# Kernel optimization log

Hardware: AMD Instinct MI355X
Metric: run time of the kernel (lower is better)

Reference implementation:

```python
import jax, jax.numpy as jnp
import numpy as np

B, T, D = 4, 4096, 1024
H = 16
DK = D // H
EPS = 1e-6


def _phi(x):
    return jax.nn.elu(x) + 1.0


def setup_inputs() -> dict:
    key = jax.random.key(0)
    ks = jax.random.split(key, 9)
    s = 1.0 / np.sqrt(D)
    return {
        "x": jax.random.normal(ks[0], (B, T, D), dtype=jnp.float32),
        "Wq": jax.random.uniform(ks[1], (D, D), jnp.float32, -s, s),
        "bq": jax.random.uniform(ks[2], (D,), jnp.float32, -s, s),
        "Wk": jax.random.uniform(ks[3], (D, D), jnp.float32, -s, s),
        "bk": jax.random.uniform(ks[4], (D,), jnp.float32, -s, s),
        "Wv": jax.random.uniform(ks[5], (D, D), jnp.float32, -s, s),
        "bv": jax.random.uniform(ks[6], (D,), jnp.float32, -s, s),
        "Wo": jax.random.uniform(ks[7], (D, D), jnp.float32, -s, s),
        "bo": jax.random.uniform(ks[8], (D,), jnp.float32, -s, s),
    }


def reference(x, Wq, bq, Wk, bk, Wv, bv, Wo, bo):
    Bq, Tq, _ = x.shape

    def heads(y):  # [B,T,D] -> [B,H,T,DK]
        return y.reshape(Bq, Tq, H, DK).transpose(0, 2, 1, 3)

    q = _phi(heads(x @ Wq.T + bq))
    k = _phi(heads(x @ Wk.T + bk))
    v = heads(x @ Wv.T + bv)

    # associative KV summary: [B,H,DK,DK]
    kv = jnp.einsum("bhtd,bhtm->bhdm", k, v)
    # normalizer: q . (sum_t k + eps), then +eps, reciprocal
    z = 1.0 / (jnp.einsum("bhtd,bhd->bht", q, k.sum(axis=2) + EPS) + EPS)
    out = jnp.einsum("bhtd,bhdm,bht->bhtm", q, kv, z)

    out = out.transpose(0, 2, 1, 3).reshape(Bq, Tq, -1)  # [B,T,D]
    return out @ Wo.T + bo
```

## Files before the change

kernel.cpp:

```cpp
#include <hip/hip_runtime.h>
#include <cstdint>
#include <cstddef>

typedef unsigned short u16;
typedef __bf16 bf16x8 __attribute__((ext_vector_type(8)));
typedef float  f32x4  __attribute__((ext_vector_type(4)));
typedef u16    u16x8v __attribute__((ext_vector_type(8)));
typedef u16    u16x4  __attribute__((ext_vector_type(4)));

#define EPS 1e-6f

__device__ __forceinline__ u16 f2bf(float f) {
  union { float f; unsigned int u; } v; v.f = f;
  unsigned int u = v.u + 0x7FFFu + ((v.u >> 16) & 1u);
  return (u16)(u >> 16);
}
__device__ __forceinline__ float bf2f(u16 h) {
  union { unsigned int u; float f; } v; v.u = ((unsigned int)h) << 16;
  return v.f;
}
__device__ __forceinline__ void async16(const void* g, void* l) {
  __builtin_amdgcn_global_load_lds(
      (const __attribute__((address_space(1))) void*)g,
      (__attribute__((address_space(3))) void*)l, 16, 0, 0);
}

__global__ __launch_bounds__(256) void cvt_all_kernel(
    const float* __restrict__ x,
    const float* __restrict__ w0, const float* __restrict__ w1,
    const float* __restrict__ w2, const float* __restrict__ w3,
    u16* __restrict__ xb, u16* __restrict__ o0, u16* __restrict__ o1,
    u16* __restrict__ o2, u16* __restrict__ o3) {
  const int gb = blockIdx.x;
  const float* in;
  u16* out;
  int i;
  if (gb < 8192) {
    in = x; out = xb; i = gb * 256 + threadIdx.x;
  } else {
    const int wb = gb - 8192;
    in  = (wb < 512) ? w0 : (wb < 1024) ? w1 : (wb < 1536) ? w2 : w3;
    out = (wb < 512) ? o0 : (wb < 1024) ? o1 : (wb < 1536) ? o2 : o3;
    i = (wb & 511) * 256 + threadIdx.x;
  }
  const float4* p = (const float4*)in;
  float4 a = p[2 * (size_t)i], b = p[2 * (size_t)i + 1];
  u16x8v o;
  o[0] = f2bf(a.x); o[1] = f2bf(a.y); o[2] = f2bf(a.z); o[3] = f2bf(a.w);
  o[4] = f2bf(b.x); o[5] = f2bf(b.y); o[6] = f2bf(b.z); o[7] = f2bf(b.w);
  *(u16x8v*)(out + 8 * (size_t)i) = o;
}

template <int MODE>
__global__ __launch_bounds__(512) void gemm8g(
    const u16* __restrict__ A, const u16* __restrict__ Bw,
    const float* __restrict__ bias0, const float* __restrict__ bias1,
    const float* __restrict__ bias2,
    u16* __restrict__ O0, u16* __restrict__ O1, u16* __restrict__ O2,
    float* __restrict__ Of, int K) {
  __shared__ u16 sA[2][256 * 64];
  __shared__ u16 sB[2][256 * 64];

  const int tid = threadIdx.x, wave = tid >> 6, lane = tid & 63;
  const int bm = blockIdx.x * 256, bn = blockIdx.y * 256;
  const int wmh = (wave >> 2) * 64;
  const int wq  = (wave & 3) * 32;
  const int l15 = lane & 15, l4 = lane >> 4, l7 = lane & 7;

  f32x4 acc[8][4] = {};

  const int trow = tid >> 3;
  const int sch8 = ((tid & 7) ^ (trow & 7)) * 8;

#define STG_A(buf, qm, s, kt)                                                 \
  async16(A + (size_t)(bm + (s)*128 + (qm)*64 + trow) * K + (kt) + sch8,      \
          &sA[buf][(((qm)*128 + (s)*64) + wave * 8) * 64])
#define STG_B(buf, qn, s, kt)                                                 \
  async16(Bw + (size_t)(bn + ((s)*2 + (trow >> 5)) * 64 + (qn)*32 +           \
                        (trow & 31)) * K + (kt) + sch8,                       \
          &sB[buf][(((qn)*128 + (s)*64) + wave * 8) * 64])

  bf16x8 af[4][2], bq[2][2];

#define RD_A(buf, qm)                                                         \
  _Pragma("unroll") for (int m = 0; m < 4; m++)                               \
    _Pragma("unroll") for (int kk = 0; kk < 2; kk++)                          \
      af[m][kk] = *(const bf16x8*)&sA[buf][((qm)*128 + wmh + m * 16 + l15) * 64 \
                                           + ((kk * 4 + l4) ^ l7) * 8];
#define RD_B(buf, qn)                                                         \
  _Pragma("unroll") for (int f = 0; f < 2; f++)                               \
    _Pragma("unroll") for (int kk = 0; kk < 2; kk++)                          \
      bq[f][kk] = *(const bf16x8*)&sB[buf][((qn)*128 + wq + f * 16 + l15) * 64 \
                                           + ((kk * 4 + l4) ^ l7) * 8];

#define WAITV_(n) asm volatile("s_waitcnt vmcnt(" #n ")" ::: "memory")
#define WAITV(n) WAITV_(n)

#define PH_(qm, qn, W)                                                        \
  __builtin_amdgcn_s_setprio(1);                                              \
  _Pragma("unroll") for (int kk = 0; kk < 2; kk++)                            \
    _Pragma("unroll") for (int m = 0; m < 4; m++)                             \
      _Pragma("unroll") for (int n = 0; n < 2; n++)                           \
        acc[(qm)*4 + m][(qn)*2 + n] = __builtin_amdgcn_mfma_f32_16x16x32_bf16(\
            af[m][kk], bq[n][kk], acc[(qm)*4 + m][(qn)*2 + n], 0, 0, 0);      \
  __builtin_amdgcn_s_setprio(0);                                              \
  asm volatile("s_waitcnt vmcnt(" #W ") lgkmcnt(0)" ::: "memory");            \
  __builtin_amdgcn_s_barrier();                                               \
  asm volatile("" ::: "memory");
#define PH(qm, qn, W) PH_(qm, qn, W)

#define ITER8(kO, kE2, kO2, FULL, W0, W1, W2, W3, W4, W5, W6, W7)             \
  RD_A(0, 0); RD_B(0, 0);                                                     \
  STG_B(1, 0, 0, kO); STG_B(1, 0, 1, kO);                \
  PH(0, 0, W0);                                                               \
  RD_B(0, 1);                                                                 \
  if (FULL) { STG_A(0, 0, 0, kE2); STG_A(0, 0, 1, kE2); }          \
  PH(0, 1, W1);                                                               \
  RD_A(0, 1);                                                                 \
  if (FULL) { STG_B(0, 1, 0, kE2); STG_B(0, 1, 1, kE2); }          \
  PH(1, 1, W2);                                                               \
  RD_B(0, 0);                                                                 \
  if (FULL) { STG_A(0, 1, 0, kE2); STG_A(0, 1, 1, kE2); }          \
  PH(1, 0, W3);                                                               \
  RD_A(1, 0); RD_B(1, 0);                                                     \
  if (FULL) { STG_B(0, 0, 0, kE2); STG_B(0, 0, 1, kE2); }          \
  PH(0, 0, W4);                                                               \
  RD_B(1, 1);                                                                 \
  if (FULL) { STG_A(1, 0, 0, kO2); STG_A(1, 0, 1, kO2); }          \
  PH(0, 1, W5);                                                               \
  RD_A(1, 1);                                                                 \
  if (FULL) { STG_B(1, 1, 0, kO2); STG_B(1, 1, 1, kO2); }          \
  PH(1, 1, W6);                                                               \
  RD_B(1, 0);                                                                 \
  if (FULL) { STG_A(1, 1, 0, kO2); STG_A(1, 1, 1, kO2); }          \
  PH(1, 0, W7);

  STG_A(0, 0, 0, 0);  STG_A(0, 0, 1, 0);
  STG_B(0, 0, 0, 0);  STG_B(0, 0, 1, 0);
  STG_B(0, 1, 0, 0);  STG_B(0, 1, 1, 0);
  STG_A(0, 1, 0, 0);  STG_A(0, 1, 1, 0);
  STG_A(1, 0, 0, 64); STG_A(1, 0, 1, 64);
  STG_B(1, 1, 0, 64); STG_B(1, 1, 1, 64);
  STG_A(1, 1, 0, 64); STG_A(1, 1, 1, 64);
  WAITV(10);
  __builtin_amdgcn_s_barrier();
  asm volatile("" ::: "memory");

  const int NT = K >> 6;
  const int NI = NT >> 1;
  ITER8(64, 128, 192, true, 10, 10, 12, 6, 12, 12, 12, 6);
  for (int i = 1; i < NI - 1; ++i) {
    const int kO  = (2 * i + 1) * 64;
    const int kE2 = (2 * i + 2) * 64;
    const int kO2 = (2 * i + 3) * 64;
    ITER8(kO, kE2, kO2, true, 12, 12, 12, 6, 12, 12, 12, 6);
  }
  ITER8((NT - 1) * 64, 0, 0, false, 12, 12, 12, 0, 0, 0, 0, 0);
#undef STG_A
#undef STG_B
#undef RD_A
#undef RD_B
#undef WAITV
#undef WAITV_
#undef PH
#undef PH_
#undef ITER8

  const int wm = wmh * 2;
  const int wn = (wave & 3) * 64;
  const int r0 = l4 * 4, cc = l15;
  if constexpr (MODE == 1) {
    const int mat = blockIdx.y >> 2;
    u16* outp = (mat == 0) ? O0 : (mat == 1) ? O1 : O2;
    const float* bias = (mat == 0) ? bias0 : (mat == 1) ? bias1 : bias2;
    const int act = (mat < 2);
    const int colb = (blockIdx.y & 3) * 256;
    float bvv[4];
#pragma unroll
    for (int ni = 0; ni < 4; ni++) bvv[ni] = bias[colb + wn + ni * 16 + cc];
#pragma unroll
    for (int mi = 0; mi < 8; mi++) {
#pragma unroll
      for (int j = 0; j < 4; j++) {
        const int row = bm + wm + mi * 16 + r0 + j;
#pragma unroll
        for (int ni = 0; ni < 4; ni++) {
          const int col = colb + wn + ni * 16 + cc;
          float val = acc[mi][ni][j] + bvv[ni];
          if (act) val = (val > 0.f) ? (val + 1.f) : __expf(val);
          outp[(size_t)row * 1024 + col] = f2bf(val);
        }
      }
    }
  } else {
    float bvv[4];
#pragma unroll
    for (int ni = 0; ni < 4; ni++) bvv[ni] = bias0[bn + wn + ni * 16 + cc];
#pragma unroll
    for (int mi = 0; mi < 8; mi++) {
#pragma unroll
      for (int j = 0; j < 4; j++) {
        const int row = bm + wm + mi * 16 + r0 + j;
#pragma unroll
        for (int ni = 0; ni < 4; ni++) {
          const int col = bn + wn + ni * 16 + cc;
          Of[(size_t)row * 1024 + col] = acc[mi][ni][j] + bvv[ni];
        }
      }
    }
  }
}

__global__ __launch_bounds__(256) void kv_mfma_kernel(
    const u16* __restrict__ Kb, const u16* __restrict__ Vb,
    float* __restrict__ kv_part, float* __restrict__ ksum_part) {
  const int bh = blockIdx.y;
  const int chunk = blockIdx.x;
  const int b = bh >> 4, h = bh & 15;
  const int tid = threadIdx.x, wave = tid >> 6, lane = tid & 63;

  __shared__ u16 sKT[64 * 64];
  __shared__ u16 sVT[64 * 64];

  f32x4 acc[4] = {};
  f32x4 accs[4] = {};

  union { u16x8v u; bf16x8 b; } uo;
#pragma unroll
  for (int e = 0; e < 8; e++) uo.u[e] = 0x3F80;
  const bf16x8 ones = uo.b;

  const int half = tid >> 7;
  const int j    = tid & 127;
  const int tg   = j >> 3;
  const int dg   = j & 7;
  const u16* src = half ? Vb : Kb;
  u16* dst = half ? sVT : sKT;
  const int colb = (4 * tg + 8 * dg) & 63;

  const size_t rowBase = (size_t)b * 4096 + (size_t)chunk * 512;
  const size_t gbase = (rowBase + 4 * tg) * 1024 + (size_t)h * 64 + dg * 8;

  u16x8v pre[2][4];
#pragma unroll
  for (int s = 0; s < 4; s++)
    pre[0][s] = *(const u16x8v*)(src + gbase + (size_t)s * 1024);

#pragma unroll
  for (int st = 0; st < 8; st++) {
    const int cb = st & 1;
    __syncthreads();
#pragma unroll
    for (int e = 0; e < 8; e++) {
      u16x4 w;
      w[0] = pre[cb][0][e]; w[1] = pre[cb][1][e];
      w[2] = pre[cb][2][e]; w[3] = pre[cb][3][e];
      *(u16x4*)&dst[(dg * 8 + e) * 64 + colb] = w;
    }
    if (st + 1 < 8) {
      const size_t nb = gbase + (size_t)(st + 1) * 64 * 1024;
#pragma unroll
      for (int s = 0; s < 4; s++)
        pre[cb ^ 1][s] = *(const u16x8v*)(src + nb + (size_t)s * 1024);
    }
    __syncthreads();

#pragma unroll
    for (int kst = 0; kst < 2; kst++) {
      const int q8 = kst * 32 + (lane >> 4) * 8;
      bf16x8 bfrag;
      {
        const int rr = wave * 16 + (lane & 15);
        const int c = (q8 + 8 * (rr >> 3)) & 63;
        bfrag = *(const bf16x8*)&sVT[rr * 64 + c];
      }
#pragma unroll
      for (int i = 0; i < 4; i++) {
        const int rr = i * 16 + (lane & 15);
        const int c = (q8 + 8 * (rr >> 3)) & 63;
        const bf16x8 afrag = *(const bf16x8*)&sKT[rr * 64 + c];
        acc[i] = __builtin_amdgcn_mfma_f32_16x16x32_bf16(afrag, bfrag, acc[i], 0, 0, 0);
        if (wave == 0)
          accs[i] = __builtin_amdgcn_mfma_f32_16x16x32_bf16(afrag, ones, accs[i], 0, 0, 0);
      }
    }
  }

  const int r0 = (lane >> 4) * 4, cc = lane & 15;
  float* kvp = kv_part + ((size_t)chunk * 64 + bh) * 4096;
#pragma unroll
  for (int i = 0; i < 4; i++)
#pragma unroll
    for (int jj = 0; jj < 4; jj++)
      kvp[(size_t)(i * 16 + r0 + jj) * 64 + wave * 16 + cc] = acc[i][jj];
  if (wave == 0 && cc == 0) {
#pragma unroll
    for (int i = 0; i < 4; i++)
#pragma unroll
      for (int jj = 0; jj < 4; jj++)
        ksum_part[((size_t)chunk * 64 + bh) * 64 + i * 16 + r0 + jj] = accs[i][jj];
  }
}

__global__ __launch_bounds__(256) void kv_reduce_kernel(
    const float* __restrict__ kv_part, const float* __restrict__ ksum_part,
    u16* __restrict__ kvbf, float* __restrict__ ksum) {
  const int bh = blockIdx.x;
  const int tid = threadIdx.x;
#pragma unroll
  for (int it = 0; it < 4; it++) {
    const int idx = it * 1024 + tid * 4;
    float4 s = {0.f, 0.f, 0.f, 0.f};
#pragma unroll
    for (int c = 0; c < 8; c++) {
      const float4 p = *(const float4*)&kv_part[((size_t)c * 64 + bh) * 4096 + idx];
      s.x += p.x; s.y += p.y; s.z += p.z; s.w += p.w;
    }
    u16x4 o;
    o[0] = f2bf(s.x); o[1] = f2bf(s.y); o[2] = f2bf(s.z); o[3] = f2bf(s.w);
    *(u16x4*)&kvbf[(size_t)bh * 4096 + idx] = o;
  }
  if (tid < 64) {
    float s = 0.f;
#pragma unroll
    for (int c = 0; c < 8; c++)
      s += ksum_part[((size_t)c * 64 + bh) * 64 + tid];
    ksum[(size_t)bh * 64 + tid] = s;
  }
}

#define QST 80
__global__ __launch_bounds__(256) void attn_apply_kernel(
    const u16* __restrict__ Qb, const u16* __restrict__ kvbf,
    const float* __restrict__ ksum, u16* __restrict__ attn) {
  const int bh = blockIdx.y;
  const int t4 = blockIdx.x;
  const int b = bh >> 4, h = bh & 15;
  const int tid = threadIdx.x, wave = tid >> 6, lane = tid & 63;

  __shared__ u16 skvT[64 * QST];
  __shared__ u16 sq[64 * QST];
  __shared__ float sz[64];
  __shared__ float sks[64];
  __shared__ float szp[256];

  if (tid < 64) sks[tid] = ksum[(size_t)bh * 64 + tid] + EPS;
  const u16* kvp = kvbf + (size_t)bh * 4096;
  for (int i = tid; i < 4096; i += 256) {
    const int dd = i >> 6, mm = i & 63;
    skvT[mm * QST + dd] = kvp[i];
  }

  const size_t qbase0 = ((size_t)b * 4096 + (size_t)t4 * 256) * 1024 + h * 64;

  for (int st = 0; st < 4; ++st) {
    const size_t qbase = qbase0 + (size_t)st * 64 * 1024;
    __syncthreads();
    for (int i = tid; i < 4096; i += 256) {
      const int r = i >> 6, dd = i & 63;
      sq[r * QST + dd] = Qb[qbase + (size_t)r * 1024 + dd];
    }
    __syncthreads();

    {
      const int zr = tid & 63, zg = tid >> 6;
      float pz = 0.f;
#pragma unroll
      for (int jj = 0; jj < 16; jj++) {
        const int dd = zg * 16 + jj;
        pz += bf2f(sq[zr * QST + dd]) * sks[dd];
      }
      szp[zg * 64 + zr] = pz;
    }
    __syncthreads();
    if (tid < 64)
      sz[tid] = 1.f / (szp[tid] + szp[64 + tid] + szp[128 + tid] + szp[192 + tid] + EPS);
    __syncthreads();

    f32x4 acc[4] = {};
#pragma unroll
    for (int ks2 = 0; ks2 < 2; ks2++) {
      const bf16x8 a = *(const bf16x8*)&sq[(wave * 16 + (lane & 15)) * QST + ks2 * 32 + (lane >> 4) * 8];
#pragma unroll
      for (int ni = 0; ni < 4; ni++) {
        const bf16x8 bv = *(const bf16x8*)&skvT[(ni * 16 + (lane & 15)) * QST + ks2 * 32 + (lane >> 4) * 8];
        acc[ni] = __builtin_amdgcn_mfma_f32_16x16x32_bf16(a, bv, acc[ni], 0, 0, 0);
      }
    }

    const int r0 = (lane >> 4) * 4, cc = lane & 15;
#pragma unroll
    for (int ni = 0; ni < 4; ni++) {
#pragma unroll
      for (int j = 0; j < 4; j++) {
        const int r = wave * 16 + r0 + j;
        const int c = ni * 16 + cc;
        const float val = acc[ni][j] * sz[r];
        attn[qbase + (size_t)r * 1024 + c] = f2bf(val);
      }
    }
  }
}

extern "C" void kernel_launch(void* const* d_in, const int* in_sizes, int n_in,
                              void* d_out, int out_size, void* d_ws, size_t ws_size,
                              hipStream_t stream) {
  (void)in_sizes; (void)n_in; (void)out_size; (void)ws_size;
  const float* x  = (const float*)d_in[0];
  const float* Wq = (const float*)d_in[1];
  const float* bq = (const float*)d_in[2];
  const float* Wk = (const float*)d_in[3];
  const float* bk = (const float*)d_in[4];
  const float* Wv = (const float*)d_in[5];
  const float* bv = (const float*)d_in[6];
  const float* Wo = (const float*)d_in[7];
  const float* bo = (const float*)d_in[8];

  char* ws = (char*)d_ws;
  u16* xb    = (u16*)ws;  ws += 33554432;
  u16* wqkvb = (u16*)ws;  ws += 6291456;
  u16* wob   = (u16*)ws;  ws += 2097152;
  u16* Vb    = (u16*)ws;  ws += 33554432;
  u16* attn  = (u16*)ws;  ws += 33554432;
  float* kv_part   = (float*)ws; ws += 8388608;
  float* ksum_part = (float*)ws; ws += 131072;
  u16*   kvbf      = (u16*)ws;   ws += 524288;
  float* ksum      = (float*)ws; ws += 16384;

  u16* Qb = (u16*)d_out;
  u16* Kb = Qb + 16777216;

  cvt_all_kernel<<<10240, 256, 0, stream>>>(x, Wq, Wk, Wv, Wo,
                                            xb, wqkvb, wqkvb + 1048576,
                                            wqkvb + 2097152, wob);

  gemm8g<1><<<dim3(64, 12), 512, 0, stream>>>(
      xb, wqkvb, bq, bk, bv, Qb, Kb, Vb, nullptr, 1024);

  kv_mfma_kernel<<<dim3(8, 64), dim3(256), 0, stream>>>(Kb, Vb, kv_part, ksum_part);
  kv_reduce_kernel<<<64, 256, 0, stream>>>(kv_part, ksum_part, kvbf, ksum);
  attn_apply_kernel<<<dim3(16, 64), dim3(256), 0, stream>>>(Qb, kvbf, ksum, attn);

  gemm8g<0><<<dim3(64, 4), 512, 0, stream>>>(
      attn, wob, bo, nullptr, nullptr, nullptr, nullptr, nullptr,
      (float*)d_out, 1024);
}
```

Baseline: 313.1 us.

## Restructure GEMM main loop into four phases with full-width B fragments

The bf16 GEMM used by the QKV and output projections now loads all four B fragments per wave at once and runs each phase across the full N width. This halves the number of barrier-separated phases per K-pair from eight to four and regroups the async global-to-LDS staging and vmcnt waits to match. It aims to cut barrier and LDS re-read overhead, at the cost of more live registers for B fragments and a more fragile hand-tuned wait-count schedule.

```diff
diff --git a/kernel.cpp b/kernel.cpp
--- a/kernel.cpp
+++ b/kernel.cpp
@@ -52,7 +52,7 @@
 }
 
 template <int MODE>
-__global__ __launch_bounds__(512) void gemm8g(
+__global__ __launch_bounds__(512) void gemm4r(
     const u16* __restrict__ A, const u16* __restrict__ Bw,
     const float* __restrict__ bias0, const float* __restrict__ bias1,
     const float* __restrict__ bias2,
@@ -80,91 +80,90 @@
                         (trow & 31)) * K + (kt) + sch8,                       \
           &sB[buf][(((qn)*128 + (s)*64) + wave * 8) * 64])
 
-  bf16x8 af[4][2], bq[2][2];
+  bf16x8 af[4][2], bq[4][2];
 
 #define RD_A(buf, qm)                                                         \
   _Pragma("unroll") for (int m = 0; m < 4; m++)                               \
     _Pragma("unroll") for (int kk = 0; kk < 2; kk++)                          \
       af[m][kk] = *(const bf16x8*)&sA[buf][((qm)*128 + wmh + m * 16 + l15) * 64 \
                                            + ((kk * 4 + l4) ^ l7) * 8];
-#define RD_B(buf, qn)                                                         \
-  _Pragma("unroll") for (int f = 0; f < 2; f++)                               \
+#define RD_B(buf)                                                             \
+  _Pragma("unroll") for (int nf = 0; nf < 4; nf++)                            \
     _Pragma("unroll") for (int kk = 0; kk < 2; kk++)                          \
-      bq[f][kk] = *(const bf16x8*)&sB[buf][((qn)*128 + wq + f * 16 + l15) * 64 \
-                                           + ((kk * 4 + l4) ^ l7) * 8];
+      bq[nf][kk] = *(const bf16x8*)&sB[buf][((nf >> 1) * 128 + wq +           \
+                                            (nf & 1) * 16 + l15) * 64 +       \
+                                           ((kk * 4 + l4) ^ l7) * 8];
 
 #define WAITV_(n) asm volatile("s_waitcnt vmcnt(" #n ")" ::: "memory")
 #define WAITV(n) WAITV_(n)
 
-#define PH_(qm, qn, W)                                                        \
-  __builtin_amdgcn_s_setprio(1);                                              \
+#define PH_EXEC_(qm, W)                                                       \
   _Pragma("unroll") for (int kk = 0; kk < 2; kk++)                            \
     _Pragma("unroll") for (int m = 0; m < 4; m++)                             \
-      _Pragma("unroll") for (int n = 0; n < 2; n++)                           \
-        acc[(qm)*4 + m][(qn)*2 + n] = __builtin_amdgcn_mfma_f32_16x16x32_bf16(\
-            af[m][kk], bq[n][kk], acc[(qm)*4 + m][(qn)*2 + n], 0, 0, 0);      \
-  __builtin_amdgcn_s_setprio(0);                                              \
+      _Pragma("unroll") for (int nf = 0; nf < 4; nf++)                        \
+        acc[(qm)*4 + m][nf] = __builtin_amdgcn_mfma_f32_16x16x32_bf16(        \
+            af[m][kk], bq[nf][kk], acc[(qm)*4 + m][nf], 0, 0, 0);             \
   asm volatile("s_waitcnt vmcnt(" #W ") lgkmcnt(0)" ::: "memory");            \
   __builtin_amdgcn_s_barrier();                                               \
   asm volatile("" ::: "memory");
-#define PH(qm, qn, W) PH_(qm, qn, W)
-
-#define ITER8(kO, kE2, kO2, FULL, W0, W1, W2, W3, W4, W5, W6, W7)             \
-  RD_A(0, 0); RD_B(0, 0);                                                     \
-  STG_B(1, 0, 0, kO); STG_B(1, 0, 1, kO);                \
-  PH(0, 0, W0);                                                               \
-  RD_B(0, 1);                                                                 \
-  if (FULL) { STG_A(0, 0, 0, kE2); STG_A(0, 0, 1, kE2); }          \
-  PH(0, 1, W1);                                                               \
+#define PH_EXEC(qm, W) PH_EXEC_(qm, W)
+
+#define ITER_BODY(kO, kE2, kO2, hasT2, hasT3, W0, W1, W2, W3)                 \
+                  \
+  RD_B(0); RD_A(0, 0);                                                        \
+  STG_A(1, 1, 0, kO); STG_A(1, 1, 1, kO);                                     \
+  PH_EXEC(0, W0);                                                             \
+                                      \
   RD_A(0, 1);                                                                 \
-  if (FULL) { STG_B(0, 1, 0, kE2); STG_B(0, 1, 1, kE2); }          \
-  PH(1, 1, W2);                                                               \
-  RD_B(0, 0);                                                                 \
-  if (FULL) { STG_A(0, 1, 0, kE2); STG_A(0, 1, 1, kE2); }          \
-  PH(1, 0, W3);                                                               \
-  RD_A(1, 0); RD_B(1, 0);                                                     \
-  if (FULL) { STG_B(0, 0, 0, kE2); STG_B(0, 0, 1, kE2); }          \
-  PH(0, 0, W4);                                                               \
-  RD_B(1, 1);                                                                 \
-  if (FULL) { STG_A(1, 0, 0, kO2); STG_A(1, 0, 1, kO2); }          \
-  PH(0, 1, W5);                                                               \
+  if (hasT2) {                                                                \
+    STG_B(0, 0, 0, kE2); STG_B(0, 0, 1, kE2);                                 \
+    STG_B(0, 1, 0, kE2); STG_B(0, 1, 1, kE2);                                 \
+    STG_A(0, 0, 0, kE2); STG_A(0, 0, 1, kE2);                                 \
+  }                                                                           \
+  PH_EXEC(1, W1);                                                             \
+                             \
+  RD_B(1); RD_A(1, 0);                                                        \
+  if (hasT2) { STG_A(0, 1, 0, kE2); STG_A(0, 1, 1, kE2); }                    \
+  PH_EXEC(0, W2);                                                             \
+                                      \
   RD_A(1, 1);                                                                 \
-  if (FULL) { STG_B(1, 1, 0, kO2); STG_B(1, 1, 1, kO2); }          \
-  PH(1, 1, W6);                                                               \
-  RD_B(1, 0);                                                                 \
-  if (FULL) { STG_A(1, 1, 0, kO2); STG_A(1, 1, 1, kO2); }          \
-  PH(1, 0, W7);
-
+  if (hasT3) {                                                                \
+    STG_B(1, 0, 0, kO2); STG_B(1, 0, 1, kO2);                                 \
+    STG_B(1, 1, 0, kO2); STG_B(1, 1, 1, kO2);                                 \
+    STG_A(1, 0, 0, kO2); STG_A(1, 0, 1, kO2);                                 \
+  }                                                                           \
+  PH_EXEC(1, W3);
+
+  STG_B(0, 0, 0, 0);  STG_B(0, 0, 1, 0);  STG_B(0, 1, 0, 0);  STG_B(0, 1, 1, 0);
   STG_A(0, 0, 0, 0);  STG_A(0, 0, 1, 0);
-  STG_B(0, 0, 0, 0);  STG_B(0, 0, 1, 0);
-  STG_B(0, 1, 0, 0);  STG_B(0, 1, 1, 0);
   STG_A(0, 1, 0, 0);  STG_A(0, 1, 1, 0);
+  STG_B(1, 0, 0, 64); STG_B(1, 0, 1, 64); STG_B(1, 1, 0, 64); STG_B(1, 1, 1, 64);
   STG_A(1, 0, 0, 64); STG_A(1, 0, 1, 64);
-  STG_B(1, 1, 0, 64); STG_B(1, 1, 1, 64);
-  STG_A(1, 1, 0, 64); STG_A(1, 1, 1, 64);
-  WAITV(10);
+  WAITV(6);
   __builtin_amdgcn_s_barrier();
   asm volatile("" ::: "memory");
 
   const int NT = K >> 6;
   const int NI = NT >> 1;
-  ITER8(64, 128, 192, true, 10, 10, 12, 6, 12, 12, 12, 6);
-  for (int i = 1; i < NI - 1; ++i) {
+  for (int i = 0; i < NI - 1; ++i) {
     const int kO  = (2 * i + 1) * 64;
     const int kE2 = (2 * i + 2) * 64;
     const int kO2 = (2 * i + 3) * 64;
-    ITER8(kO, kE2, kO2, true, 12, 12, 12, 6, 12, 12, 12, 6);
-  }
-  ITER8((NT - 1) * 64, 0, 0, false, 12, 12, 12, 0, 0, 0, 0, 0);
+    ITER_BODY(kO, kE2, kO2, true, true, 8, 8, 8, 8);
+  }
+  {
+    const int kO = (NT - 1) * 64;
+    ITER_BODY(kO, 0, 0, false, false, 8, 2, 0, 0);
+  }
 #undef STG_A
 #undef STG_B
 #undef RD_A
 #undef RD_B
 #undef WAITV
 #undef WAITV_
-#undef PH
-#undef PH_
-#undef ITER8
+#undef PH_EXEC
+#undef PH_EXEC_
+#undef ITER_BODY
 
   const int wm = wmh * 2;
   const int wn = (wave & 3) * 64;
@@ -434,14 +433,14 @@
                                             xb, wqkvb, wqkvb + 1048576,
                                             wqkvb + 2097152, wob);
 
-  gemm8g<1><<<dim3(64, 12), 512, 0, stream>>>(
+  gemm4r<1><<<dim3(64, 12), 512, 0, stream>>>(
       xb, wqkvb, bq, bk, bv, Qb, Kb, Vb, nullptr, 1024);
 
   kv_mfma_kernel<<<dim3(8, 64), dim3(256), 0, stream>>>(Kb, Vb, kv_part, ksum_part);
   kv_reduce_kernel<<<64, 256, 0, stream>>>(kv_part, ksum_part, kvbf, ksum);
   attn_apply_kernel<<<dim3(16, 64), dim3(256), 0, stream>>>(Qb, kvbf, ksum, attn);
 
-  gemm8g<0><<<dim3(64, 4), 512, 0, stream>>>(
+  gemm4r<0><<<dim3(64, 4), 512, 0, stream>>>(
       attn, wob, bo, nullptr, nullptr, nullptr, nullptr, nullptr,
       (float*)d_out, 1024);
 }
```

Measured after the change: 295.7 us. -5.6%, faster.
